# Kernel optimization log

Hardware: AMD Instinct MI355X
Metric: run time of the kernel (lower is better)

The kernel has to match this reference:

```python
import jax, jax.numpy as jnp
import numpy as np

NUM_MOLS = 16384          # num_original_mols (fixed segment count)
TOTAL_KEYS = 1048576      # total fragments in batch (~64 per molecule)
QUERY_DIM = 128
KEY_DIM = 128
HIDDEN = 128              # attention_hidden_dim


def setup_inputs() -> dict:
    key = jax.random.key(0)
    k1, k2, k3, k4, k5 = jax.random.split(key, 5)
    query_batch = jax.random.normal(k1, (NUM_MOLS, QUERY_DIM), dtype=jnp.float32)
    key_batch = jax.random.normal(k2, (TOTAL_KEYS, KEY_DIM), dtype=jnp.float32)
    WQ = jax.random.normal(k3, (HIDDEN, QUERY_DIM), dtype=jnp.float32) * 0.05
    WK = jax.random.normal(k4, (HIDDEN, KEY_DIM), dtype=jnp.float32) * 0.05
    original_mol_idx_for_keys = jnp.sort(
        jax.random.randint(k5, (TOTAL_KEYS,), 0, NUM_MOLS, dtype=jnp.int64.dtype if hasattr(jnp.int64, 'dtype') else jnp.int64)
    ).astype(jnp.int32)
    return {
        "query_batch": query_batch,
        "key_batch": key_batch,
        "WQ": WQ,
        "WK": WK,
        "original_mol_idx_for_keys": original_mol_idx_for_keys,
    }


def reference(query_batch, key_batch, WQ, WK, original_mol_idx_for_keys):
    idx = original_mol_idx_for_keys
    # Dense projections (torch Linear, no bias): x @ W^T
    Q_proj = query_batch @ WQ.T                      # [num_mols, H]
    K_proj = key_batch @ WK.T                        # [total_keys, H]
    # Gather query rows per key, elementwise dot-product score
    scores = jnp.sum(Q_proj[idx] * K_proj, axis=1) / jnp.sqrt(
        jnp.asarray(HIDDEN, dtype=K_proj.dtype)
    )                                                # [total_keys]
    # scatter_softmax over variable-length segments (stable)
    seg_max = jax.ops.segment_max(scores, idx, num_segments=NUM_MOLS)
    ex = jnp.exp(scores - seg_max[idx])
    seg_sum = jax.ops.segment_sum(ex, idx, num_segments=NUM_MOLS)
    weights = ex / seg_sum[idx]
    return (weights, scores)
```

## Files before the change

kernel.cpp:

```cpp
#include <hip/hip_runtime.h>
#include <hip/hip_bf16.h>

#define QUERY_DIM 128
#define HIDDEN 128

typedef float f32x4 __attribute__((ext_vector_type(4)));

__device__ __forceinline__ float dot4(f32x4 a, f32x4 b) {
    return a.x * b.x + a.y * b.y + a.z * b.z + a.w * b.w;
}

__global__ __launch_bounds__(256) void combo_kernel(const float* __restrict__ WQ,
                                                    const float* __restrict__ WK,
                                                    float* __restrict__ W,
                                                    const int* __restrict__ idx,
                                                    int* __restrict__ start,
                                                    int nmols, int total) {
    int b = blockIdx.x;
    int t = threadIdx.x;
    if (b < 64) {
        int e = b * 2 + (t >> 7);
        int d = t & 127;
        float acc = 0.f;
#pragma unroll 8
        for (int h = 0; h < HIDDEN; ++h) {
            acc += WQ[h * QUERY_DIM + e] * WK[h * 128 + d];
        }
        W[e * 128 + d] = acc;
    } else {
        int m = (b - 64) * 256 + t;
        if (m > nmols) return;
        if (m == nmols) { start[m] = total; return; }
        int lo = 0, hi = total;
        while (lo < hi) {
            int mid = (lo + hi) >> 1;
            if (idx[mid] < m) lo = mid + 1; else hi = mid;
        }
        start[m] = lo;
    }
}

__global__ __launch_bounds__(256) void qproj_kernel(const float* __restrict__ Q,
                                                    const float* __restrict__ W,
                                                    float* __restrict__ R, int nmols) {
    __shared__ float wl[64 * 128];
    __shared__ float ql[16 * 128];
    int t = threadIdx.x;
    int c = t & 127;
    int g = t >> 7;
    long row0 = (long)blockIdx.x * 16;

    for (int i = t * 4; i < 16 * 128; i += 256 * 4) {
        *(float4*)&ql[i] = *(const float4*)&Q[row0 * QUERY_DIM + i];
    }

    float acc[8] = {0.f, 0.f, 0.f, 0.f, 0.f, 0.f, 0.f, 0.f};

    for (int half = 0; half < 2; ++half) {
        __syncthreads();
        for (int i = t * 4; i < 64 * 128; i += 256 * 4) {
            *(float4*)&wl[i] = *(const float4*)&W[half * 64 * 128 + i];
        }
        __syncthreads();
        for (int d = 0; d < 64; d += 4) {
            float w0 = wl[(d + 0) * 128 + c];
            float w1 = wl[(d + 1) * 128 + c];
            float w2 = wl[(d + 2) * 128 + c];
            float w3 = wl[(d + 3) * 128 + c];
            int dg = half * 64 + d;
#pragma unroll
            for (int r = 0; r < 8; ++r) {
                f32x4 q = *(const f32x4*)&ql[(g * 8 + r) * 128 + dg];
                acc[r] += q.x * w0 + q.y * w1 + q.z * w2 + q.w * w3;
            }
        }
    }
#pragma unroll
    for (int r = 0; r < 8; ++r) {
        long row = row0 + g * 8 + r;
        if (row < nmols) R[row * 128 + c] = acc[r];
    }
}

__global__ __launch_bounds__(256) void fused_kernel(const float* __restrict__ K,
                                                    const float* __restrict__ R,
                                                    const int* __restrict__ start,
                                                    float* __restrict__ weights,
                                                    float* scores,
                                                    int nmols) {
    const int lane = threadIdx.x & 63;
    const int half = lane >> 5;
    const int hl = lane & 31;
    const int wave = (blockIdx.x * 256 + threadIdx.x) >> 6;
    const int nwaves = gridDim.x * 4;
    const float sc = 0.08838834764831845f;

    for (int s = wave; s < nmols; s += nwaves) {
        int s0 = start[s], s1 = start[s + 1];
        if (s0 >= s1) continue;

        f32x4 rfrag = *((const f32x4*)(R + (long)s * 128) + hl);

        float mx = -__builtin_inff();
        int kb = s0;
        for (; kb + 8 <= s1; kb += 8) {
            long k = kb + half;
            const f32x4* p0 = (const f32x4*)(K + (k + 0) * 128) + hl;
            const f32x4* p1 = (const f32x4*)(K + (k + 2) * 128) + hl;
            const f32x4* p2 = (const f32x4*)(K + (k + 4) * 128) + hl;
            const f32x4* p3 = (const f32x4*)(K + (k + 6) * 128) + hl;
            f32x4 a0 = __builtin_nontemporal_load(p0);
            f32x4 a1 = __builtin_nontemporal_load(p1);
            f32x4 a2 = __builtin_nontemporal_load(p2);
            f32x4 a3 = __builtin_nontemporal_load(p3);
            float v0 = dot4(a0, rfrag);
            float v1 = dot4(a1, rfrag);
            float v2 = dot4(a2, rfrag);
            float v3 = dot4(a3, rfrag);
#pragma unroll
            for (int off = 16; off > 0; off >>= 1) {
                v0 += __shfl_xor(v0, off, 64);
                v1 += __shfl_xor(v1, off, 64);
                v2 += __shfl_xor(v2, off, 64);
                v3 += __shfl_xor(v3, off, 64);
            }
            v0 *= sc; v1 *= sc; v2 *= sc; v3 *= sc;
            if (hl == 0) {
                scores[k + 0] = v0;
                scores[k + 2] = v1;
                scores[k + 4] = v2;
                scores[k + 6] = v3;
            }
            mx = fmaxf(mx, fmaxf(fmaxf(v0, v1), fmaxf(v2, v3)));
        }
        for (long k = kb + half; k < s1; k += 2) {
            f32x4 kv = __builtin_nontemporal_load((const f32x4*)(K + k * 128) + hl);
            float v = dot4(kv, rfrag);
#pragma unroll
            for (int off = 16; off > 0; off >>= 1) v += __shfl_xor(v, off, 64);
            v *= sc;
            if (hl == 0) scores[k] = v;
            mx = fmaxf(mx, v);
        }
        mx = fmaxf(mx, __shfl_xor(mx, 32, 64));

        asm volatile("s_waitcnt vmcnt(0)" ::: "memory");

        float sum = 0.f;
        for (int i = s0 + lane; i < s1; i += 64) sum += __expf(scores[i] - mx);
#pragma unroll
        for (int off = 32; off > 0; off >>= 1) sum += __shfl_xor(sum, off, 64);
        float inv = 1.0f / sum;

        for (int i = s0 + lane; i < s1; i += 64)
            weights[i] = __expf(scores[i] - mx) * inv;
    }
}

extern "C" void kernel_launch(void* const* d_in, const int* in_sizes, int n_in,
                              void* d_out, int out_size, void* d_ws, size_t ws_size,
                              hipStream_t stream) {
    const float* Q   = (const float*)d_in[0];
    const float* K   = (const float*)d_in[1];
    const float* WQ  = (const float*)d_in[2];
    const float* WK  = (const float*)d_in[3];
    const int*   idx = (const int*)d_in[4];

    const int nmols = in_sizes[0] / QUERY_DIM;
    const int total = in_sizes[4];

    float* weights = (float*)d_out;
    float* scores  = (float*)d_out + total;

    char* ws = (char*)d_ws;
    float* W        = (float*)ws;
    int*   segstart = (int*)(ws + 65536);
    float* R        = (float*)(ws + 65536 + 131072);

    int segblocks = (nmols + 1 + 255) / 256;
    combo_kernel<<<64 + segblocks, 256, 0, stream>>>(WQ, WK, W, idx, segstart, nmols, total);
    qproj_kernel<<<(nmols + 15) / 16, 256, 0, stream>>>(Q, W, R, nmols);
    fused_kernel<<<2048, 256, 0, stream>>>(K, R, segstart, weights, scores, nmols);
}
```

Measured before the change: 137.7 us.

## Prefetch next key tile, use online softmax, fix two segments per wave

The main loop now double-buffers K loads, issuing the next 8-row group before computing dot products on the current one. It also keeps a running online max and sum, so the separate pass that re-reads scores to build the exponent sum is gone, and the two wave halves are merged with a rescaled combine. The grid-stride loop over segments becomes a fixed two segments per wave. That mapping covers all segments only when the grid size times 8 is at least nmols, and it adds extra exp work and register pressure inside the hot loop.

Result: no change. 138.5 us (+0.6%).

```diff
diff --git a/kernel.cpp b/kernel.cpp
--- a/kernel.cpp
+++ b/kernel.cpp
@@ -92,27 +92,39 @@
     const int half = lane >> 5;
     const int hl = lane & 31;
     const int wave = (blockIdx.x * 256 + threadIdx.x) >> 6;
-    const int nwaves = gridDim.x * 4;
     const float sc = 0.08838834764831845f;
 
-    for (int s = wave; s < nmols; s += nwaves) {
+    for (int si = 0; si < 2; ++si) {
+        int s = wave * 2 + si;
+        if (s >= nmols) break;
         int s0 = start[s], s1 = start[s + 1];
         if (s0 >= s1) continue;
 
         f32x4 rfrag = *((const f32x4*)(R + (long)s * 128) + hl);
 
         float mx = -__builtin_inff();
+        float sum = 0.f;
         int kb = s0;
-        for (; kb + 8 <= s1; kb += 8) {
+
+        f32x4 a0, a1, a2, a3;
+        bool have = (kb + 8 <= s1);
+        if (have) {
             long k = kb + half;
-            const f32x4* p0 = (const f32x4*)(K + (k + 0) * 128) + hl;
-            const f32x4* p1 = (const f32x4*)(K + (k + 2) * 128) + hl;
-            const f32x4* p2 = (const f32x4*)(K + (k + 4) * 128) + hl;
-            const f32x4* p3 = (const f32x4*)(K + (k + 6) * 128) + hl;
-            f32x4 a0 = __builtin_nontemporal_load(p0);
-            f32x4 a1 = __builtin_nontemporal_load(p1);
-            f32x4 a2 = __builtin_nontemporal_load(p2);
-            f32x4 a3 = __builtin_nontemporal_load(p3);
+            a0 = __builtin_nontemporal_load((const f32x4*)(K + (k + 0) * 128) + hl);
+            a1 = __builtin_nontemporal_load((const f32x4*)(K + (k + 2) * 128) + hl);
+            a2 = __builtin_nontemporal_load((const f32x4*)(K + (k + 4) * 128) + hl);
+            a3 = __builtin_nontemporal_load((const f32x4*)(K + (k + 6) * 128) + hl);
+        }
+        while (have) {
+            bool havenext = (kb + 16 <= s1);
+            f32x4 b0, b1, b2, b3;
+            if (havenext) {
+                long kn = kb + 8 + half;
+                b0 = __builtin_nontemporal_load((const f32x4*)(K + (kn + 0) * 128) + hl);
+                b1 = __builtin_nontemporal_load((const f32x4*)(K + (kn + 2) * 128) + hl);
+                b2 = __builtin_nontemporal_load((const f32x4*)(K + (kn + 4) * 128) + hl);
+                b3 = __builtin_nontemporal_load((const f32x4*)(K + (kn + 6) * 128) + hl);
+            }
             float v0 = dot4(a0, rfrag);
             float v1 = dot4(a1, rfrag);
             float v2 = dot4(a2, rfrag);
@@ -125,13 +137,22 @@
                 v3 += __shfl_xor(v3, off, 64);
             }
             v0 *= sc; v1 *= sc; v2 *= sc; v3 *= sc;
+            long k = kb + half;
             if (hl == 0) {
                 scores[k + 0] = v0;
                 scores[k + 2] = v1;
                 scores[k + 4] = v2;
                 scores[k + 6] = v3;
             }
-            mx = fmaxf(mx, fmaxf(fmaxf(v0, v1), fmaxf(v2, v3)));
+            float bm = fmaxf(fmaxf(v0, v1), fmaxf(v2, v3));
+            float nm = fmaxf(mx, bm);
+            sum = sum * __expf(mx - nm)
+                + __expf(v0 - nm) + __expf(v1 - nm)
+                + __expf(v2 - nm) + __expf(v3 - nm);
+            mx = nm;
+            kb += 8;
+            a0 = b0; a1 = b1; a2 = b2; a3 = b3;
+            have = havenext;
         }
         for (long k = kb + half; k < s1; k += 2) {
             f32x4 kv = __builtin_nontemporal_load((const f32x4*)(K + k * 128) + hl);
@@ -140,17 +161,18 @@
             for (int off = 16; off > 0; off >>= 1) v += __shfl_xor(v, off, 64);
             v *= sc;
             if (hl == 0) scores[k] = v;
-            mx = fmaxf(mx, v);
-        }
-        mx = fmaxf(mx, __shfl_xor(mx, 32, 64));
+            float nm = fmaxf(mx, v);
+            sum = sum * __expf(mx - nm) + __expf(v - nm);
+            mx = nm;
+        }
+        float mo = __shfl_xor(mx, 32, 64);
+        float so = __shfl_xor(sum, 32, 64);
+        float nm = fmaxf(mx, mo);
+        sum = sum * __expf(mx - nm) + so * __expf(mo - nm);
+        mx = nm;
+        float inv = 1.0f / sum;
 
         asm volatile("s_waitcnt vmcnt(0)" ::: "memory");
-
-        float sum = 0.f;
-        for (int i = s0 + lane; i < s1; i += 64) sum += __expf(scores[i] - mx);
-#pragma unroll
-        for (int off = 32; off > 0; off >>= 1) sum += __shfl_xor(sum, off, 64);
-        float inv = 1.0f / sum;
 
         for (int i = s0 + lane; i < s1; i += 64)
             weights[i] = __expf(scores[i] - mx) * inv;
```

## Re-tile query projection with 4-column register blocking and regroup kernels

Applied to the files above, without the earlier changes.

Splits the WQ^T·WK product into its own small kernel and moves the segment-start binary search into the query-projection launch. The projection now handles 64 rows per block, and each thread computes a 4-wide column vector for 8 rows, so shared-memory tiles are reused more and results are stored as float4. The aim is fewer LDS reads per FMA and fewer, larger blocks, in exchange for more shared memory and registers per block and one extra tiny launch.

Measured after the change: 130.6 us (median of 2 runs). -5.1%, faster.

```diff
diff --git a/kernel.cpp b/kernel.cpp
--- a/kernel.cpp
+++ b/kernel.cpp
@@ -10,25 +10,29 @@
     return a.x * b.x + a.y * b.y + a.z * b.z + a.w * b.w;
 }
 
-__global__ __launch_bounds__(256) void combo_kernel(const float* __restrict__ WQ,
-                                                    const float* __restrict__ WK,
-                                                    float* __restrict__ W,
-                                                    const int* __restrict__ idx,
-                                                    int* __restrict__ start,
-                                                    int nmols, int total) {
+__global__ void wqk_kernel(const float* __restrict__ WQ,
+                           const float* __restrict__ WK,
+                           float* __restrict__ W) {
+    int e = blockIdx.x;
+    int d = threadIdx.x;
+    float acc = 0.f;
+#pragma unroll 8
+    for (int h = 0; h < HIDDEN; ++h) {
+        acc += WQ[h * QUERY_DIM + e] * WK[h * 128 + d];
+    }
+    W[e * 128 + d] = acc;
+}
+
+__global__ __launch_bounds__(256) void qproj2_kernel(const float* __restrict__ Q,
+                                                     const float* __restrict__ W,
+                                                     float* __restrict__ R,
+                                                     const int* __restrict__ idx,
+                                                     int* __restrict__ start,
+                                                     int nmols, int total, int qblocks) {
     int b = blockIdx.x;
     int t = threadIdx.x;
-    if (b < 64) {
-        int e = b * 2 + (t >> 7);
-        int d = t & 127;
-        float acc = 0.f;
-#pragma unroll 8
-        for (int h = 0; h < HIDDEN; ++h) {
-            acc += WQ[h * QUERY_DIM + e] * WK[h * 128 + d];
-        }
-        W[e * 128 + d] = acc;
-    } else {
-        int m = (b - 64) * 256 + t;
+    if (b >= qblocks) {
+        int m = (b - qblocks) * 256 + t;
         if (m > nmols) return;
         if (m == nmols) { start[m] = total; return; }
         int lo = 0, hi = total;
@@ -37,37 +41,37 @@
             if (idx[mid] < m) lo = mid + 1; else hi = mid;
         }
         start[m] = lo;
-    }
-}
-
-__global__ __launch_bounds__(256) void qproj_kernel(const float* __restrict__ Q,
-                                                    const float* __restrict__ W,
-                                                    float* __restrict__ R, int nmols) {
-    __shared__ float wl[64 * 128];
-    __shared__ float ql[16 * 128];
-    int t = threadIdx.x;
-    int c = t & 127;
-    int g = t >> 7;
-    long row0 = (long)blockIdx.x * 16;
-
-    for (int i = t * 4; i < 16 * 128; i += 256 * 4) {
-        *(float4*)&ql[i] = *(const float4*)&Q[row0 * QUERY_DIM + i];
+        return;
     }
 
-    float acc[8] = {0.f, 0.f, 0.f, 0.f, 0.f, 0.f, 0.f, 0.f};
+    __shared__ float wl[64 * 128];
+    __shared__ float ql[64 * 128];
+    const int c4 = (t & 31) * 4;
+    const int g  = t >> 5;
+    const long row0 = (long)b * 64;
 
-    for (int half = 0; half < 2; ++half) {
+    for (int i = t * 4; i < 64 * 128; i += 256 * 4) {
+        long rr = row0 + (i >> 7);
+        if (rr > nmols - 1) rr = nmols - 1;
+        *(f32x4*)&ql[i] = *(const f32x4*)&Q[rr * 128 + (i & 127)];
+    }
+
+    f32x4 acc[8];
+#pragma unroll
+    for (int r = 0; r < 8; ++r) acc[r] = (f32x4){0.f, 0.f, 0.f, 0.f};
+
+    for (int hf = 0; hf < 2; ++hf) {
         __syncthreads();
         for (int i = t * 4; i < 64 * 128; i += 256 * 4) {
-            *(float4*)&wl[i] = *(const float4*)&W[half * 64 * 128 + i];
+            *(f32x4*)&wl[i] = *(const f32x4*)&W[hf * 64 * 128 + i];
         }
         __syncthreads();
         for (int d = 0; d < 64; d += 4) {
-            float w0 = wl[(d + 0) * 128 + c];
-            float w1 = wl[(d + 1) * 128 + c];
-            float w2 = wl[(d + 2) * 128 + c];
-            float w3 = wl[(d + 3) * 128 + c];
-            int dg = half * 64 + d;
+            f32x4 w0 = *(const f32x4*)&wl[(d + 0) * 128 + c4];
+            f32x4 w1 = *(const f32x4*)&wl[(d + 1) * 128 + c4];
+            f32x4 w2 = *(const f32x4*)&wl[(d + 2) * 128 + c4];
+            f32x4 w3 = *(const f32x4*)&wl[(d + 3) * 128 + c4];
+            int dg = hf * 64 + d;
 #pragma unroll
             for (int r = 0; r < 8; ++r) {
                 f32x4 q = *(const f32x4*)&ql[(g * 8 + r) * 128 + dg];
@@ -78,7 +82,7 @@
 #pragma unroll
     for (int r = 0; r < 8; ++r) {
         long row = row0 + g * 8 + r;
-        if (row < nmols) R[row * 128 + c] = acc[r];
+        if (row < nmols) *(f32x4*)&R[row * 128 + c4] = acc[r];
     }
 }
 
@@ -177,8 +181,10 @@
     int*   segstart = (int*)(ws + 65536);
     float* R        = (float*)(ws + 65536 + 131072);
 
+    wqk_kernel<<<128, 128, 0, stream>>>(WQ, WK, W);
+    int qblocks  = (nmols + 63) / 64;
     int segblocks = (nmols + 1 + 255) / 256;
-    combo_kernel<<<64 + segblocks, 256, 0, stream>>>(WQ, WK, W, idx, segstart, nmols, total);
-    qproj_kernel<<<(nmols + 15) / 16, 256, 0, stream>>>(Q, W, R, nmols);
+    qproj2_kernel<<<qblocks + segblocks, 256, 0, stream>>>(Q, W, R, idx, segstart,
+                                                           nmols, total, qblocks);
     fused_kernel<<<2048, 256, 0, stream>>>(K, R, segstart, weights, scores, nmols);
 }
```
